# Kernel tuning notes

Measured on AMD Instinct MI355X. Metric: run time of the kernel, lower is better.

Reference implementation:

```python
import jax, jax.numpy as jnp
import numpy as np

B, D, C = 8192, 1024, 4096  # batch, d_model, num_clusters (all active)
EPS = 1e-12  # matches F.normalize eps


def _l2_normalize(x):
    n = jnp.linalg.norm(x, axis=-1, keepdims=True)
    return x / jnp.maximum(n, EPS)


def setup_inputs() -> dict:
    key = jax.random.key(0)
    k1, k2 = jax.random.split(key)
    embedding = jax.random.normal(k1, (B, D), dtype=jnp.float32)
    centroids = jax.random.normal(k2, (C, D), dtype=jnp.float32)  # buffer, all active
    return {"embedding": embedding, "centroids": centroids}


def reference(embedding, centroids):
    # Fused equivalent of the per-centroid Python loop:
    # cosine sim of normalized embedding vs each normalized centroid.
    emb_n = _l2_normalize(embedding)        # [B, D]
    cen_n = _l2_normalize(centroids)        # [C, D]
    sims = jnp.clip(emb_n @ cen_n.T, 0.0, 1.0)  # [B, C], per-sim clamp to [0,1]
    max_sim = jnp.max(sims, axis=-1)        # [B]
    closest = jnp.argmax(sims, axis=-1)     # [B] int
    novelty = jnp.clip(jnp.sqrt(1.0 - max_sim), 0.0, 1.0)  # [B]
    return novelty, closest
```

## Files before the change

kernel.cpp:

```cpp
#include <hip/hip_runtime.h>
#include <math.h>

#define B_ROWS 8192
#define C_COLS 4096
#define D_DIM  1024
#define EPSN   1e-12f

typedef float v4f __attribute__((ext_vector_type(4)));
typedef short v8s __attribute__((ext_vector_type(8)));

__device__ __forceinline__ unsigned short bf16_rtn(float x) {
    unsigned int u = __float_as_uint(x);
    u += 0x7fffu + ((u >> 16) & 1u);
    return (unsigned short)(u >> 16);
}

__device__ __forceinline__ bool better_vi(float v, int i, float V, int I) {
    return (v > V) || (v == V && i < I);
}

__global__ __launch_bounds__(256) void prep_kernel(
    const float* __restrict__ emb, const float* __restrict__ cen,
    unsigned short* __restrict__ Ah, unsigned short* __restrict__ Bh,
    float* __restrict__ inv_a, float* __restrict__ inv_b)
{
    const int lane = threadIdx.x & 63;
    const int wid  = blockIdx.x * 4 + (threadIdx.x >> 6);
    const float* src; unsigned short* dst; float* invp; int r;
    if (wid < B_ROWS) { src = emb; r = wid;          dst = Ah; invp = inv_a; }
    else              { src = cen; r = wid - B_ROWS; dst = Bh; invp = inv_b; }

    const float* rp = src + (size_t)r * D_DIM;
    float4 v[4];
    float ss = 0.0f;
    #pragma unroll
    for (int j = 0; j < 4; ++j) {
        v[j] = *(const float4*)(rp + (j * 64 + lane) * 4);
        ss += v[j].x * v[j].x + v[j].y * v[j].y + v[j].z * v[j].z + v[j].w * v[j].w;
    }
    #pragma unroll
    for (int off = 1; off < 64; off <<= 1) ss += __shfl_xor(ss, off, 64);

    const float iv = 1.0f / fmaxf(sqrtf(ss), EPSN);
    if (lane == 0) invp[r] = iv;

    unsigned short* dp = dst + (size_t)r * D_DIM;
    #pragma unroll
    for (int j = 0; j < 4; ++j) {
        ushort4 H;
        H.x = bf16_rtn(v[j].x * iv);
        H.y = bf16_rtn(v[j].y * iv);
        H.z = bf16_rtn(v[j].z * iv);
        H.w = bf16_rtn(v[j].w * iv);
        *(ushort4*)(dp + (j * 64 + lane) * 4) = H;
    }
}

__global__ __launch_bounds__(256, 4) void simmax_kernel(
    const unsigned short* __restrict__ Ahg, const unsigned short* __restrict__ Bhg,
    float* __restrict__ p1v, int* __restrict__ p1i,
    float* __restrict__ p2v, int* __restrict__ p2i)
{
    __shared__ unsigned short lds[2 * 8192];

    const int tid    = threadIdx.x;
    const int L      = tid & 63;
    const int w      = tid >> 6;
    const int lane15 = L & 15;
    const int quad   = L >> 4;
    const int wr     = w >> 1, wc = w & 1;
    const int row0   = blockIdx.x * 128;
    const int c0     = blockIdx.y * 128;

    const int scol = (tid & 7) ^ ((tid >> 3) & 7);
    const unsigned short* aBase = Ahg + (size_t)(row0 + (tid >> 3)) * D_DIM + scol * 8;
    const unsigned short* bBase = Bhg + (size_t)(c0   + (tid >> 3)) * D_DIM + scol * 8;

    v4f acc[4][4];
    #pragma unroll
    for (int mt = 0; mt < 4; ++mt)
        #pragma unroll
        for (int nt = 0; nt < 4; ++nt) acc[mt][nt] = (v4f)0.0f;

    int rAo[4], rBo[4];
    #pragma unroll
    for (int t = 0; t < 4; ++t) {
        rAo[t] = (wr * 64 + t * 16 + lane15) * 64;
        rBo[t] = (wc * 64 + t * 16 + lane15) * 64;
    }
    const int s7 = lane15 & 7;
    const int cq[2] = { (quad ^ s7) * 8, ((4 + quad) ^ s7) * 8 };

    for (int kc = 0; kc < D_DIM / 64; ++kc) {
        const int kb = kc * 64;
        #pragma unroll
        for (int i = 0; i < 4; ++i) {
            __builtin_amdgcn_global_load_lds(
                (const __attribute__((address_space(1))) void*)(aBase + (size_t)i * 32 * D_DIM + kb),
                (__attribute__((address_space(3))) void*)&lds[(i * 256 + w * 64) * 8], 16, 0, 0);
            __builtin_amdgcn_global_load_lds(
                (const __attribute__((address_space(1))) void*)(bBase + (size_t)i * 32 * D_DIM + kb),
                (__attribute__((address_space(3))) void*)&lds[8192 + (i * 256 + w * 64) * 8], 16, 0, 0);
        }
        __syncthreads();

        #pragma unroll
        for (int h = 0; h < 2; ++h) {
            v8s fah[4], fbh[4];
            #pragma unroll
            for (int t = 0; t < 4; ++t) {
                fah[t] = *(const v8s*)&lds[rAo[t] + cq[h]];
                fbh[t] = *(const v8s*)&lds[8192 + rBo[t] + cq[h]];
            }
            #pragma unroll
            for (int mt = 0; mt < 4; ++mt)
                #pragma unroll
                for (int nt = 0; nt < 4; ++nt)
                    acc[mt][nt] = __builtin_amdgcn_mfma_f32_16x16x32_bf16(fah[mt], fbh[nt], acc[mt][nt], 0, 0, 0);
        }
        __syncthreads();
    }

    const int pc = blockIdx.y * 2 + wc;
    #pragma unroll
    for (int mt = 0; mt < 4; ++mt) {
        #pragma unroll
        for (int r = 0; r < 4; ++r) {
            float a1v = acc[mt][0][r];
            int   a1i = c0 + wc * 64 + 0 * 16 + lane15;
            float a2v = -1e30f;
            int   a2i = 0x7fffffff;
            #pragma unroll
            for (int nt = 1; nt < 4; ++nt) {
                float v  = acc[mt][nt][r];
                int   ci = c0 + wc * 64 + nt * 16 + lane15;
                if (better_vi(v, ci, a1v, a1i))      { a2v = a1v; a2i = a1i; a1v = v; a1i = ci; }
                else if (better_vi(v, ci, a2v, a2i)) { a2v = v;   a2i = ci; }
            }
            #pragma unroll
            for (int off = 8; off; off >>= 1) {
                float b1v = __shfl_down(a1v, off, 64); int b1i = __shfl_down(a1i, off, 64);
                float b2v = __shfl_down(a2v, off, 64); int b2i = __shfl_down(a2i, off, 64);
                if (better_vi(b1v, b1i, a1v, a1i)) {
                    if (better_vi(a1v, a1i, b2v, b2i)) { a2v = a1v; a2i = a1i; }
                    else                               { a2v = b2v; a2i = b2i; }
                    a1v = b1v; a1i = b1i;
                } else if (better_vi(b1v, b1i, a2v, a2i)) {
                    a2v = b1v; a2i = b1i;
                }
            }
            if (lane15 == 0) {
                int rg = row0 + wr * 64 + mt * 16 + quad * 4 + r;
                size_t ix = (size_t)rg * 64 + pc;
                p1v[ix] = a1v; p1i[ix] = a1i;
                p2v[ix] = a2v; p2i[ix] = a2i;
            }
        }
    }
}

__global__ __launch_bounds__(256) void finalize_kernel(
    const float* __restrict__ emb, const float* __restrict__ cen,
    const float* __restrict__ inv_a, const float* __restrict__ inv_b,
    const float* __restrict__ p1v, const int* __restrict__ p1i,
    const float* __restrict__ p2v, const int* __restrict__ p2i,
    float* __restrict__ out)
{
    const int lane = threadIdx.x & 63;
    const int row  = blockIdx.x * 4 + (threadIdx.x >> 6);
    const size_t base = (size_t)row * 64 + lane;

    float v[4]; int ix[4];
    v[0] = p1v[base]; ix[0] = p1i[base];
    v[1] = p2v[base]; ix[1] = p2i[base];
    v[2] = -1e30f;    ix[2] = 0x7ffffffe;
    v[3] = -1e30f;    ix[3] = 0x7fffffff;

    #pragma unroll
    for (int off = 1; off < 64; off <<= 1) {
        float ov[4]; int oi[4];
        #pragma unroll
        for (int k = 0; k < 4; ++k) {
            ov[k] = __shfl_xor(v[k],  off, 64);
            oi[k] = __shfl_xor(ix[k], off, 64);
        }
        #pragma unroll
        for (int k = 0; k < 4; ++k) {
            float bv = ov[k]; int bi = oi[k];
            bool b0 = better_vi(bv, bi, v[0], ix[0]);
            bool b1 = better_vi(bv, bi, v[1], ix[1]);
            bool b2 = better_vi(bv, bi, v[2], ix[2]);
            bool b3 = better_vi(bv, bi, v[3], ix[3]);
            float nv3 = b2 ? v[2] : (b3 ? bv : v[3]); int ni3 = b2 ? ix[2] : (b3 ? bi : ix[3]);
            float nv2 = b1 ? v[1] : (b2 ? bv : v[2]); int ni2 = b1 ? ix[1] : (b2 ? bi : ix[2]);
            float nv1 = b0 ? v[0] : (b1 ? bv : v[1]); int ni1 = b0 ? ix[0] : (b1 ? bi : ix[1]);
            float nv0 = b0 ? bv   : v[0];             int ni0 = b0 ? bi    : ix[0];
            v[0] = nv0; ix[0] = ni0; v[1] = nv1; ix[1] = ni1;
            v[2] = nv2; ix[2] = ni2; v[3] = nv3; ix[3] = ni3;
        }
    }

    const float* er = emb + (size_t)row * D_DIM;
    const float* cr0 = cen + (size_t)ix[0] * D_DIM;
    const float* cr1 = cen + (size_t)ix[1] * D_DIM;
    const float* cr2 = cen + (size_t)ix[2] * D_DIM;
    const float* cr3 = cen + (size_t)ix[3] * D_DIM;

    float d[4] = { 0.0f, 0.0f, 0.0f, 0.0f };
    #pragma unroll
    for (int j = 0; j < 4; ++j) {
        int e = (j * 64 + lane) * 4;
        float4 ev = *(const float4*)(er  + e);
        float4 c0 = *(const float4*)(cr0 + e);
        float4 c1 = *(const float4*)(cr1 + e);
        float4 c2 = *(const float4*)(cr2 + e);
        float4 c3 = *(const float4*)(cr3 + e);
        d[0] += ev.x * c0.x + ev.y * c0.y + ev.z * c0.z + ev.w * c0.w;
        d[1] += ev.x * c1.x + ev.y * c1.y + ev.z * c1.z + ev.w * c1.w;
        d[2] += ev.x * c2.x + ev.y * c2.y + ev.z * c2.z + ev.w * c2.w;
        d[3] += ev.x * c3.x + ev.y * c3.y + ev.z * c3.z + ev.w * c3.w;
    }
    #pragma unroll
    for (int off = 1; off < 64; off <<= 1) {
        #pragma unroll
        for (int c = 0; c < 4; ++c) d[c] += __shfl_xor(d[c], off, 64);
    }

    if (lane == 0) {
        const float ia = inv_a[row];
        float m = -1e30f; int ci = 0x7fffffff;
        #pragma unroll
        for (int c = 0; c < 4; ++c) {
            float s = d[c] * ia * inv_b[ix[c]];
            if (better_vi(s, ix[c], m, ci)) { m = s; ci = ix[c]; }
        }
        if (m <= 0.0f) ci = 0;
        float ms = fminf(fmaxf(m, 0.0f), 1.0f);
        out[row]          = fminf(fmaxf(sqrtf(1.0f - ms), 0.0f), 1.0f);
        out[B_ROWS + row] = (float)ci;
    }
}

extern "C" void kernel_launch(void* const* d_in, const int* in_sizes, int n_in,
                              void* d_out, int out_size, void* d_ws, size_t ws_size,
                              hipStream_t stream)
{
    const float* emb = (const float*)d_in[0];
    const float* cen = (const float*)d_in[1];
    float* out = (float*)d_out;

    unsigned short* Ahp = (unsigned short*)d_ws;
    unsigned short* Bhp = Ahp + (size_t)B_ROWS * D_DIM;
    float* inv_a = (float*)(Bhp + (size_t)C_COLS * D_DIM);
    float* inv_b = inv_a + B_ROWS;
    float* p1v   = inv_b + C_COLS;
    int*   p1i   = (int*)(p1v + (size_t)64 * B_ROWS);
    float* p2v   = (float*)(p1i + (size_t)64 * B_ROWS);
    int*   p2i   = (int*)(p2v + (size_t)64 * B_ROWS);

    prep_kernel<<<(B_ROWS + C_COLS) / 4, 256, 0, stream>>>(emb, cen, Ahp, Bhp, inv_a, inv_b);

    dim3 grid(B_ROWS / 128, C_COLS / 128);
    simmax_kernel<<<grid, 256, 0, stream>>>(Ahp, Bhp, p1v, p1i, p2v, p2i);

    finalize_kernel<<<B_ROWS / 4, 256, 0, stream>>>(emb, cen, inv_a, inv_b,
                                                    p1v, p1i, p2v, p2i, out);
}
```

Baseline: 203.2 us.

## Fuse finalize into simmax via last-block-per-row-tile atomic counter

Removes the separate finalize kernel launch. Each simmax block increments a per-row-tile counter, and the last of the 32 column blocks for a row tile reduces the partial top-2 candidates and does the fp32 rescoring for its 128 rows. The counters are zeroed in the prep kernel. This saves a launch and its tail, but puts the finalize work on a few late blocks, whose 4 waves each handle 32 rows in sequence, and adds threadfence and atomic overhead to every block.

```diff
diff --git a/kernel.cpp b/kernel.cpp
--- a/kernel.cpp
+++ b/kernel.cpp
@@ -22,8 +22,11 @@
 __global__ __launch_bounds__(256) void prep_kernel(
     const float* __restrict__ emb, const float* __restrict__ cen,
     unsigned short* __restrict__ Ah, unsigned short* __restrict__ Bh,
-    float* __restrict__ inv_a, float* __restrict__ inv_b)
+    float* __restrict__ inv_a, float* __restrict__ inv_b,
+    int* __restrict__ cnt)
 {
+    if (blockIdx.x == 0 && threadIdx.x < 64) cnt[threadIdx.x] = 0;
+
     const int lane = threadIdx.x & 63;
     const int wid  = blockIdx.x * 4 + (threadIdx.x >> 6);
     const float* src; unsigned short* dst; float* invp; int r;
@@ -58,10 +61,14 @@
 
 __global__ __launch_bounds__(256, 4) void simmax_kernel(
     const unsigned short* __restrict__ Ahg, const unsigned short* __restrict__ Bhg,
+    const float* __restrict__ emb, const float* __restrict__ cen,
+    const float* __restrict__ inv_a, const float* __restrict__ inv_b,
     float* __restrict__ p1v, int* __restrict__ p1i,
-    float* __restrict__ p2v, int* __restrict__ p2i)
+    float* __restrict__ p2v, int* __restrict__ p2i,
+    int* __restrict__ cnt, float* __restrict__ out)
 {
     __shared__ unsigned short lds[2 * 8192];
+    __shared__ int lastFlag;
 
     const int tid    = threadIdx.x;
     const int L      = tid & 63;
@@ -157,87 +164,90 @@
             }
         }
     }
-}
-
-__global__ __launch_bounds__(256) void finalize_kernel(
-    const float* __restrict__ emb, const float* __restrict__ cen,
-    const float* __restrict__ inv_a, const float* __restrict__ inv_b,
-    const float* __restrict__ p1v, const int* __restrict__ p1i,
-    const float* __restrict__ p2v, const int* __restrict__ p2i,
-    float* __restrict__ out)
-{
-    const int lane = threadIdx.x & 63;
-    const int row  = blockIdx.x * 4 + (threadIdx.x >> 6);
-    const size_t base = (size_t)row * 64 + lane;
-
-    float v[4]; int ix[4];
-    v[0] = p1v[base]; ix[0] = p1i[base];
-    v[1] = p2v[base]; ix[1] = p2i[base];
-    v[2] = -1e30f;    ix[2] = 0x7ffffffe;
-    v[3] = -1e30f;    ix[3] = 0x7fffffff;
-
-    #pragma unroll
-    for (int off = 1; off < 64; off <<= 1) {
-        float ov[4]; int oi[4];
-        #pragma unroll
-        for (int k = 0; k < 4; ++k) {
-            ov[k] = __shfl_xor(v[k],  off, 64);
-            oi[k] = __shfl_xor(ix[k], off, 64);
-        }
-        #pragma unroll
-        for (int k = 0; k < 4; ++k) {
-            float bv = ov[k]; int bi = oi[k];
-            bool b0 = better_vi(bv, bi, v[0], ix[0]);
-            bool b1 = better_vi(bv, bi, v[1], ix[1]);
-            bool b2 = better_vi(bv, bi, v[2], ix[2]);
-            bool b3 = better_vi(bv, bi, v[3], ix[3]);
-            float nv3 = b2 ? v[2] : (b3 ? bv : v[3]); int ni3 = b2 ? ix[2] : (b3 ? bi : ix[3]);
-            float nv2 = b1 ? v[1] : (b2 ? bv : v[2]); int ni2 = b1 ? ix[1] : (b2 ? bi : ix[2]);
-            float nv1 = b0 ? v[0] : (b1 ? bv : v[1]); int ni1 = b0 ? ix[0] : (b1 ? bi : ix[1]);
-            float nv0 = b0 ? bv   : v[0];             int ni0 = b0 ? bi    : ix[0];
-            v[0] = nv0; ix[0] = ni0; v[1] = nv1; ix[1] = ni1;
-            v[2] = nv2; ix[2] = ni2; v[3] = nv3; ix[3] = ni3;
-        }
-    }
-
-    const float* er = emb + (size_t)row * D_DIM;
-    const float* cr0 = cen + (size_t)ix[0] * D_DIM;
-    const float* cr1 = cen + (size_t)ix[1] * D_DIM;
-    const float* cr2 = cen + (size_t)ix[2] * D_DIM;
-    const float* cr3 = cen + (size_t)ix[3] * D_DIM;
-
-    float d[4] = { 0.0f, 0.0f, 0.0f, 0.0f };
-    #pragma unroll
-    for (int j = 0; j < 4; ++j) {
-        int e = (j * 64 + lane) * 4;
-        float4 ev = *(const float4*)(er  + e);
-        float4 c0 = *(const float4*)(cr0 + e);
-        float4 c1 = *(const float4*)(cr1 + e);
-        float4 c2 = *(const float4*)(cr2 + e);
-        float4 c3 = *(const float4*)(cr3 + e);
-        d[0] += ev.x * c0.x + ev.y * c0.y + ev.z * c0.z + ev.w * c0.w;
-        d[1] += ev.x * c1.x + ev.y * c1.y + ev.z * c1.z + ev.w * c1.w;
-        d[2] += ev.x * c2.x + ev.y * c2.y + ev.z * c2.z + ev.w * c2.w;
-        d[3] += ev.x * c3.x + ev.y * c3.y + ev.z * c3.z + ev.w * c3.w;
-    }
-    #pragma unroll
-    for (int off = 1; off < 64; off <<= 1) {
-        #pragma unroll
-        for (int c = 0; c < 4; ++c) d[c] += __shfl_xor(d[c], off, 64);
-    }
-
-    if (lane == 0) {
-        const float ia = inv_a[row];
-        float m = -1e30f; int ci = 0x7fffffff;
-        #pragma unroll
-        for (int c = 0; c < 4; ++c) {
-            float s = d[c] * ia * inv_b[ix[c]];
-            if (better_vi(s, ix[c], m, ci)) { m = s; ci = ix[c]; }
-        }
-        if (m <= 0.0f) ci = 0;
-        float ms = fminf(fmaxf(m, 0.0f), 1.0f);
-        out[row]          = fminf(fmaxf(sqrtf(1.0f - ms), 0.0f), 1.0f);
-        out[B_ROWS + row] = (float)ci;
+
+    __syncthreads();
+    if (tid == 0) {
+        __threadfence();
+        int old = atomicAdd(cnt + blockIdx.x, 1);
+        lastFlag = ((old & 31) == 31) ? 1 : 0;
+    }
+    __syncthreads();
+    if (!lastFlag) return;
+    __threadfence();
+
+    for (int rr = 0; rr < 32; ++rr) {
+        const int row = row0 + w * 32 + rr;
+        const size_t base = (size_t)row * 64 + L;
+
+        float v[4]; int ix[4];
+        v[0] = p1v[base]; ix[0] = p1i[base];
+        v[1] = p2v[base]; ix[1] = p2i[base];
+        v[2] = -1e30f;    ix[2] = 0x7ffffffe;
+        v[3] = -1e30f;    ix[3] = 0x7fffffff;
+
+        #pragma unroll
+        for (int off = 1; off < 64; off <<= 1) {
+            float ov[4]; int oi[4];
+            #pragma unroll
+            for (int k = 0; k < 4; ++k) {
+                ov[k] = __shfl_xor(v[k],  off, 64);
+                oi[k] = __shfl_xor(ix[k], off, 64);
+            }
+            #pragma unroll
+            for (int k = 0; k < 4; ++k) {
+                float bv = ov[k]; int bi = oi[k];
+                bool b0 = better_vi(bv, bi, v[0], ix[0]);
+                bool b1 = better_vi(bv, bi, v[1], ix[1]);
+                bool b2 = better_vi(bv, bi, v[2], ix[2]);
+                bool b3 = better_vi(bv, bi, v[3], ix[3]);
+                float nv3 = b2 ? v[2] : (b3 ? bv : v[3]); int ni3 = b2 ? ix[2] : (b3 ? bi : ix[3]);
+                float nv2 = b1 ? v[1] : (b2 ? bv : v[2]); int ni2 = b1 ? ix[1] : (b2 ? bi : ix[2]);
+                float nv1 = b0 ? v[0] : (b1 ? bv : v[1]); int ni1 = b0 ? ix[0] : (b1 ? bi : ix[1]);
+                float nv0 = b0 ? bv   : v[0];             int ni0 = b0 ? bi    : ix[0];
+                v[0] = nv0; ix[0] = ni0; v[1] = nv1; ix[1] = ni1;
+                v[2] = nv2; ix[2] = ni2; v[3] = nv3; ix[3] = ni3;
+            }
+        }
+
+        const float* er  = emb + (size_t)row * D_DIM;
+        const float* cr0 = cen + (size_t)ix[0] * D_DIM;
+        const float* cr1 = cen + (size_t)ix[1] * D_DIM;
+        const float* cr2 = cen + (size_t)ix[2] * D_DIM;
+        const float* cr3 = cen + (size_t)ix[3] * D_DIM;
+
+        float d[4] = { 0.0f, 0.0f, 0.0f, 0.0f };
+        #pragma unroll
+        for (int j = 0; j < 4; ++j) {
+            int e = (j * 64 + L) * 4;
+            float4 ev = *(const float4*)(er  + e);
+            float4 c0 = *(const float4*)(cr0 + e);
+            float4 c1 = *(const float4*)(cr1 + e);
+            float4 c2 = *(const float4*)(cr2 + e);
+            float4 c3 = *(const float4*)(cr3 + e);
+            d[0] += ev.x * c0.x + ev.y * c0.y + ev.z * c0.z + ev.w * c0.w;
+            d[1] += ev.x * c1.x + ev.y * c1.y + ev.z * c1.z + ev.w * c1.w;
+            d[2] += ev.x * c2.x + ev.y * c2.y + ev.z * c2.z + ev.w * c2.w;
+            d[3] += ev.x * c3.x + ev.y * c3.y + ev.z * c3.z + ev.w * c3.w;
+        }
+        #pragma unroll
+        for (int off = 1; off < 64; off <<= 1) {
+            #pragma unroll
+            for (int c = 0; c < 4; ++c) d[c] += __shfl_xor(d[c], off, 64);
+        }
+
+        if (L == 0) {
+            const float ia = inv_a[row];
+            float m = -1e30f; int ci = 0x7fffffff;
+            #pragma unroll
+            for (int c = 0; c < 4; ++c) {
+                float s = d[c] * ia * inv_b[ix[c]];
+                if (better_vi(s, ix[c], m, ci)) { m = s; ci = ix[c]; }
+            }
+            if (m <= 0.0f) ci = 0;
+            float ms = fminf(fmaxf(m, 0.0f), 1.0f);
+            out[row]          = fminf(fmaxf(sqrtf(1.0f - ms), 0.0f), 1.0f);
+            out[B_ROWS + row] = (float)ci;
+        }
     }
 }
 
@@ -257,12 +267,12 @@
     int*   p1i   = (int*)(p1v + (size_t)64 * B_ROWS);
     float* p2v   = (float*)(p1i + (size_t)64 * B_ROWS);
     int*   p2i   = (int*)(p2v + (size_t)64 * B_ROWS);
-
-    prep_kernel<<<(B_ROWS + C_COLS) / 4, 256, 0, stream>>>(emb, cen, Ahp, Bhp, inv_a, inv_b);
+    int*   cnt   = p2i + (size_t)64 * B_ROWS;
+
+    prep_kernel<<<(B_ROWS + C_COLS) / 4, 256, 0, stream>>>(emb, cen, Ahp, Bhp,
+                                                           inv_a, inv_b, cnt);
 
     dim3 grid(B_ROWS / 128, C_COLS / 128);
-    simmax_kernel<<<grid, 256, 0, stream>>>(Ahp, Bhp, p1v, p1i, p2v, p2i);
-
-    finalize_kernel<<<B_ROWS / 4, 256, 0, stream>>>(emb, cen, inv_a, inv_b,
-                                                    p1v, p1i, p2v, p2i, out);
-}
+    simmax_kernel<<<grid, 256, 0, stream>>>(Ahp, Bhp, emb, cen, inv_a, inv_b,
+                                            p1v, p1i, p2v, p2i, cnt, out);
+}
```

New measurement: 435.2 us. +114.1%, slower.
